# Kernel tuning notes

Measured on AMD Instinct MI355X. Metric: run time of the kernel, lower is better.

Reference implementation:

```python
import jax, jax.numpy as jnp
import numpy as np

MAX = 1e10
H, DK, DV = 16, 64, 64  # heads, key_size, value_size


def setup_inputs() -> dict:
    key = jax.random.key(0)
    ks = jax.random.split(key, 8)
    B, S, D = 2, 2048, 1024
    q = jax.random.normal(ks[0], (B, S, D), dtype=jnp.float32)
    k = jax.random.normal(ks[1], (B, S, D), dtype=jnp.float32)
    v = jax.random.normal(ks[2], (B, S, D), dtype=jnp.float32)
    v_mask = jax.random.randint(ks[3], (B, S), 0, 2, dtype=jnp.int32)
    q_mask = jax.random.randint(ks[4], (B, S), 0, 2, dtype=jnp.int32)
    sc = 1.0 / np.sqrt(D)
    Wq = jax.random.normal(ks[5], (D, H * DK), dtype=jnp.float32) * sc
    Wk = jax.random.normal(ks[6], (D, H * DK), dtype=jnp.float32) * sc
    Wv = jax.random.normal(ks[7], (D, H * DV), dtype=jnp.float32) * sc
    return {"q": q, "k": k, "v": v, "v_mask": v_mask, "q_mask": q_mask,
            "Wq": Wq, "Wk": Wk, "Wv": Wv}


def reference(q, k, v, v_mask, q_mask, Wq, Wk, Wv):
    B, Sq, _ = q.shape
    Sk = k.shape[1]
    # projections -> [B, H, S, d]
    qh = (q @ Wq).reshape(B, Sq, H, DK).transpose(0, 2, 1, 3)
    kh = (k @ Wk).reshape(B, Sk, H, DK).transpose(0, 2, 1, 3)
    vh = (v @ Wv).reshape(B, Sk, H, DV).transpose(0, 2, 1, 3)
    # scores [B, H, Sq, Sk]
    a = jnp.einsum('bhqd,bhkd->bhqk', qh, kh) / np.sqrt(DK).astype(np.float32)
    # additive key-padding mask over key dim
    vm = v_mask.astype(a.dtype)
    a = a - (1.0 - vm)[:, None, None, :] * MAX
    # causal mask (band-part trick)
    causal = jnp.tril(jnp.ones((Sq, Sk), dtype=a.dtype))
    a = a - (1.0 - causal) * MAX
    a = jax.nn.softmax(a, axis=-1)
    out = jnp.einsum('bhqk,bhkd->bqhd', a, vh).reshape(B, Sq, H * DV)
    # multiplicative query-padding mask
    out = out * q_mask.astype(out.dtype)[:, :, None]
    return out
```

## Files before the change

### kernel.cpp

```cpp
#include <hip/hip_runtime.h>
#include <hip/hip_bf16.h>

#define H_    16
#define S_    2048
#define D_    1024
#define MAXV  1e10f

typedef __attribute__((ext_vector_type(8))) short short8;
typedef __attribute__((ext_vector_type(4))) float f32x4;

__device__ __forceinline__ unsigned short f2bf(float f) {
    union { float f; unsigned u; } x; x.f = f;
    unsigned r = x.u + 0x7fffu + ((x.u >> 16) & 1u);
    return (unsigned short)(r >> 16);
}
__device__ __forceinline__ float bf2f(unsigned short h) {
    union { unsigned u; float f; } x; x.u = ((unsigned)h) << 16; return x.f;
}

__global__ __launch_bounds__(256) void scan_kernel(
        const int* __restrict__ vmask, int* __restrict__ cmap,
        int* __restrict__ Jc, int* __restrict__ cumi) {
    int bb = blockIdx.x;
    const int* vm = vmask + (size_t)bb * S_;
    int t = threadIdx.x, lane = t & 63, wave = t >> 6;
    int j0 = t * 8;
    int loc[8], tot = 0;
#pragma unroll
    for (int e = 0; e < 8; e++) { loc[e] = vm[j0 + e] ? 1 : 0; tot += loc[e]; }
    int pre = tot;
#pragma unroll
    for (int d = 1; d < 64; d <<= 1) {
        int x = __shfl_up(pre, d);
        if (lane >= d) pre += x;
    }
    __shared__ int wtot[4];
    if (lane == 63) wtot[wave] = pre;
    __syncthreads();
    int wbase = 0;
    for (int w = 0; w < wave; w++) wbase += wtot[w];
    int run = wbase + pre - tot;
    for (int e = 0; e < 8; e++) {
        int j = j0 + e;
        int before = run;
        run += loc[e];
        cumi[(size_t)bb * S_ + j] = run;
        if (loc[e]) {
            cmap[(size_t)bb * S_ + j] = before;
            Jc[(size_t)bb * S_ + before] = j;
        } else {
            cmap[(size_t)bb * S_ + j] = -1;
        }
    }
    int total = wtot[0] + wtot[1] + wtot[2] + wtot[3];
    for (int c = total + t; c < S_; c += 256) Jc[(size_t)bb * S_ + c] = S_;
}

__global__ __launch_bounds__(256) void wtrans_kernel(
        const float* __restrict__ w0, const float* __restrict__ w1,
        const float* __restrict__ w2, unsigned short* __restrict__ wt) {
    const float* W = blockIdx.z == 0 ? w0 : (blockIdx.z == 1 ? w1 : w2);
    unsigned short* Wt = wt + (size_t)blockIdx.z * (D_ * D_);
    __shared__ float tile[32][33];
    int t = threadIdx.x;
    int k0 = blockIdx.y * 32, n0 = blockIdx.x * 32;
    int r = t >> 3, c4 = (t & 7) * 4;
    float4 v = *(const float4*)&W[(size_t)(k0 + r) * D_ + n0 + c4];
    tile[r][c4 + 0] = v.x; tile[r][c4 + 1] = v.y;
    tile[r][c4 + 2] = v.z; tile[r][c4 + 3] = v.w;
    __syncthreads();
    ushort4 o;
    o.x = f2bf(tile[c4 + 0][r]); o.y = f2bf(tile[c4 + 1][r]);
    o.z = f2bf(tile[c4 + 2][r]); o.w = f2bf(tile[c4 + 3][r]);
    *(ushort4*)&Wt[(size_t)(n0 + r) * D_ + k0 + c4] = o;
}

__global__ __launch_bounds__(256) void conv_kernel(
        const float* __restrict__ q, const float* __restrict__ k,
        const float* __restrict__ v, unsigned short* __restrict__ abf) {
    int z = blockIdx.y;
    const float* src = z == 0 ? q : (z == 1 ? k : v);
    unsigned short* dst = abf + (size_t)z * (4096ull * 1024);
    size_t i = ((size_t)blockIdx.x * 256 + threadIdx.x) * 8;
    float4 f1 = *(const float4*)&src[i];
    float4 f2 = *(const float4*)&src[i + 4];
    short8 o;
    o[0] = (short)f2bf(f1.x); o[1] = (short)f2bf(f1.y);
    o[2] = (short)f2bf(f1.z); o[3] = (short)f2bf(f1.w);
    o[4] = (short)f2bf(f2.x); o[5] = (short)f2bf(f2.y);
    o[6] = (short)f2bf(f2.z); o[7] = (short)f2bf(f2.w);
    *(short8*)&dst[i] = o;
}

template <bool PRE>
__global__ __launch_bounds__(256) void proj_kernel(
        const float* __restrict__ q, const float* __restrict__ k,
        const float* __restrict__ v, const unsigned short* __restrict__ abf,
        const unsigned short* __restrict__ wt, const int* __restrict__ cmap,
        unsigned short* __restrict__ Qh, unsigned short* __restrict__ Kc,
        unsigned short* __restrict__ Vtc) {
    int z = blockIdx.z;
    const float* Af = z == 0 ? q : (z == 1 ? k : v);
    const unsigned short* Ab = abf + (size_t)z * (4096ull * 1024);
    const unsigned short* Bt = wt + (size_t)z * (D_ * D_);
    int m0 = blockIdx.y * 128;
    int n0 = blockIdx.x * 128;
    __shared__ __align__(16) unsigned short As[128][72];
    __shared__ __align__(16) unsigned short Bs[128][72];
    int t = threadIdx.x;
    int wave = t >> 6, lane = t & 63, lg = lane >> 4, lr = lane & 15;
    int wr = (wave >> 1) * 64, wc = (wave & 1) * 64;
    f32x4 acc[4][4];
#pragma unroll
    for (int mi = 0; mi < 4; mi++)
#pragma unroll
        for (int ni = 0; ni < 4; ni++) acc[mi][ni] = (f32x4){0.f, 0.f, 0.f, 0.f};

    int srow = t >> 3, scol = (t & 7) * 8;
    for (int kt = 0; kt < D_ / 64; ++kt) {
        int kk0 = kt * 64;
        __syncthreads();
#pragma unroll
        for (int i = 0; i < 4; i++) {
            int row = i * 32 + srow;
            if (PRE) {
                *(short8*)&As[row][scol] =
                    *(const short8*)&Ab[(size_t)(m0 + row) * D_ + kk0 + scol];
            } else {
                float4 f1 = *(const float4*)&Af[(size_t)(m0 + row) * D_ + kk0 + scol];
                float4 f2 = *(const float4*)&Af[(size_t)(m0 + row) * D_ + kk0 + scol + 4];
                short8 o;
                o[0] = (short)f2bf(f1.x); o[1] = (short)f2bf(f1.y);
                o[2] = (short)f2bf(f1.z); o[3] = (short)f2bf(f1.w);
                o[4] = (short)f2bf(f2.x); o[5] = (short)f2bf(f2.y);
                o[6] = (short)f2bf(f2.z); o[7] = (short)f2bf(f2.w);
                *(short8*)&As[row][scol] = o;
            }
            *(short8*)&Bs[row][scol] =
                *(const short8*)&Bt[(size_t)(n0 + row) * D_ + kk0 + scol];
        }
        __syncthreads();
        short8 af[4][2], bq[4][2];
#pragma unroll
        for (int mi = 0; mi < 4; mi++)
#pragma unroll
            for (int kh = 0; kh < 2; kh++)
                af[mi][kh] = *(const short8*)&As[wr + mi * 16 + lr][kh * 32 + lg * 8];
#pragma unroll
        for (int ni = 0; ni < 4; ni++)
#pragma unroll
            for (int kh = 0; kh < 2; kh++)
                bq[ni][kh] = *(const short8*)&Bs[wc + ni * 16 + lr][kh * 32 + lg * 8];
        __builtin_amdgcn_s_setprio(1);
#pragma unroll
        for (int kh = 0; kh < 2; kh++)
#pragma unroll
            for (int mi = 0; mi < 4; mi++)
#pragma unroll
                for (int ni = 0; ni < 4; ni++)
                    acc[mi][ni] = __builtin_amdgcn_mfma_f32_16x16x32_bf16(
                        af[mi][kh], bq[ni][kh], acc[mi][ni], 0, 0, 0);
        __builtin_amdgcn_s_setprio(0);
    }
    if (z == 0) {
#pragma unroll
        for (int mi = 0; mi < 4; mi++) {
#pragma unroll
            for (int ni = 0; ni < 4; ni++) {
                int col = n0 + wc + ni * 16 + lr;
                int hh = col >> 6, dk = col & 63;
#pragma unroll
                for (int rr = 0; rr < 4; rr++) {
                    int m = m0 + wr + mi * 16 + lg * 4 + rr;
                    int bb = m >> 11, s = m & (S_ - 1);
                    Qh[(((size_t)(bb * H_ + hh)) * S_ + s) * 64 + dk] =
                        f2bf(acc[mi][ni][rr]);
                }
            }
        }
    } else {
        int cm_[4][4], bb_[4][4];
#pragma unroll
        for (int mi = 0; mi < 4; mi++)
#pragma unroll
            for (int rr = 0; rr < 4; rr++) {
                int m = m0 + wr + mi * 16 + lg * 4 + rr;
                int bb = m >> 11, s = m & (S_ - 1);
                bb_[mi][rr] = bb;
                cm_[mi][rr] = cmap[(size_t)bb * S_ + s];
            }
#pragma unroll
        for (int mi = 0; mi < 4; mi++) {
#pragma unroll
            for (int ni = 0; ni < 4; ni++) {
                int col = n0 + wc + ni * 16 + lr;
                int hh = col >> 6, dd = col & 63;
#pragma unroll
                for (int rr = 0; rr < 4; rr++) {
                    int c = cm_[mi][rr];
                    if (c < 0) continue;
                    int bb = bb_[mi][rr];
                    if (z == 1)
                        Kc[(((size_t)(bb * H_ + hh)) * S_ + c) * 64 + dd] =
                            f2bf(acc[mi][ni][rr]);
                    else
                        Vtc[(((size_t)(bb * H_ + hh)) * 64 + dd) * S_ + c] =
                            f2bf(acc[mi][ni][rr]);
                }
            }
        }
    }
}

__global__ __launch_bounds__(256) void attn_kernel(
        const unsigned short* __restrict__ Qh, const unsigned short* __restrict__ Kc,
        const unsigned short* __restrict__ Vtc, const int* __restrict__ Jc,
        const int* __restrict__ cumi, const int* __restrict__ qmask,
        float* __restrict__ out) {
    int pair = blockIdx.x, hh = blockIdx.y, bb = blockIdx.z;
    const unsigned short* Qp = Qh + ((size_t)(bb * H_ + hh)) * S_ * 64;
    const unsigned short* Kp = Kc + ((size_t)(bb * H_ + hh)) * S_ * 64;
    const unsigned short* Vp = Vtc + ((size_t)(bb * H_ + hh)) * 64 * S_;
    const int* Jb = Jc + (size_t)bb * S_;
    int t = threadIdx.x, wave = t >> 6, lane = t & 63, lg = lane >> 4, lr = lane & 15;
    __shared__ __align__(16) unsigned short Ks[64 * 64];
    __shared__ __align__(16) unsigned short Vs[64 * 64];
    __shared__ __align__(16) unsigned short Pl[4][16][72];

    for (int half = 0; half < 2; half++) {
        int qt = half ? (31 - pair) : pair;
        int q0 = qt * 64 + wave * 16;
        int nc = cumi[(size_t)bb * S_ + qt * 64 + 63];
        int nt = (nc + 63) >> 6;
        short8 qf[2];
#pragma unroll
        for (int kh = 0; kh < 2; kh++)
            qf[kh] = *(const short8*)&Qp[(size_t)(q0 + lr) * 64 + kh * 32 + lg * 8];
        f32x4 oacc[4];
#pragma unroll
        for (int ni = 0; ni < 4; ni++) oacc[ni] = (f32x4){0.f, 0.f, 0.f, 0.f};
        float m_run[4], l_run[4];
        int qrow[4];
#pragma unroll
        for (int rr = 0; rr < 4; rr++) {
            m_run[rr] = -__builtin_inff(); l_run[rr] = 0.f;
            qrow[rr] = q0 + lg * 4 + rr;
        }

        for (int kt = 0; kt < nt; ++kt) {
            int kv0 = kt * 64;
            __syncthreads();
#pragma unroll
            for (int i = 0; i < 2; i++) {
                int off = i * 4096 + t * 16;
                int row = off >> 7, colb = off & 127;
                int csw = colb ^ ((row & 7) << 4);
                short8 kkv = *(const short8*)((const char*)Kp + (size_t)(kv0 + row) * 128 + csw);
                short8 vvv = *(const short8*)((const char*)Vp + (size_t)row * 4096 + kv0 * 2 + csw);
                *(short8*)((char*)Ks + off) = kkv;
                *(short8*)((char*)Vs + off) = vvv;
            }
            __syncthreads();
            f32x4 sacc[4];
#pragma unroll
            for (int ni = 0; ni < 4; ni++) sacc[ni] = (f32x4){0.f, 0.f, 0.f, 0.f};
            __builtin_amdgcn_s_setprio(1);
#pragma unroll
            for (int ni = 0; ni < 4; ni++) {
                int row = ni * 16 + lr;
#pragma unroll
                for (int kh = 0; kh < 2; kh++) {
                    int cb = (kh * 64 + lg * 16) ^ ((row & 7) << 4);
                    short8 kf = *(const short8*)((const char*)Ks + row * 128 + cb);
                    sacc[ni] = __builtin_amdgcn_mfma_f32_16x16x32_bf16(qf[kh], kf, sacc[ni], 0, 0, 0);
                }
            }
            __builtin_amdgcn_s_setprio(0);
            float sv[4][4];
#pragma unroll
            for (int ni = 0; ni < 4; ni++) {
                int jo = Jb[kv0 + ni * 16 + lr];
#pragma unroll
                for (int rr = 0; rr < 4; rr++) {
                    float s = sacc[ni][rr] * 0.125f;
                    if (jo > qrow[rr]) s -= MAXV;
                    sv[ni][rr] = s;
                }
            }
            float scl[4];
#pragma unroll
            for (int rr = 0; rr < 4; rr++) {
                float a = fmaxf(fmaxf(sv[0][rr], sv[1][rr]), fmaxf(sv[2][rr], sv[3][rr]));
#pragma unroll
                for (int d = 1; d < 16; d <<= 1) a = fmaxf(a, __shfl_xor(a, d));
                float mn = fmaxf(m_run[rr], a);
                scl[rr] = __expf(m_run[rr] - mn);
                m_run[rr] = mn;
            }
            float pw[4][4], ps[4];
#pragma unroll
            for (int rr = 0; rr < 4; rr++) ps[rr] = 0.f;
#pragma unroll
            for (int ni = 0; ni < 4; ni++)
#pragma unroll
                for (int rr = 0; rr < 4; rr++) {
                    pw[ni][rr] = __expf(sv[ni][rr] - m_run[rr]);
                    ps[rr] += pw[ni][rr];
                }
#pragma unroll
            for (int rr = 0; rr < 4; rr++) {
#pragma unroll
                for (int d = 1; d < 16; d <<= 1) ps[rr] += __shfl_xor(ps[rr], d);
                l_run[rr] = l_run[rr] * scl[rr] + ps[rr];
            }
#pragma unroll
            for (int ni = 0; ni < 4; ni++)
#pragma unroll
                for (int rr = 0; rr < 4; rr++) oacc[ni][rr] *= scl[rr];
#pragma unroll
            for (int ni = 0; ni < 4; ni++)
#pragma unroll
                for (int rr = 0; rr < 4; rr++)
                    Pl[wave][lg * 4 + rr][ni * 16 + lr] = f2bf(pw[ni][rr]);
            short8 pa[2];
#pragma unroll
            for (int kh = 0; kh < 2; kh++)
                pa[kh] = *(const short8*)&Pl[wave][lr][kh * 32 + lg * 8];
            __builtin_amdgcn_s_setprio(1);
#pragma unroll
            for (int ni = 0; ni < 4; ni++) {
                int rowd = ni * 16 + lr;
#pragma unroll
                for (int kh = 0; kh < 2; kh++) {
                    int cb = (kh * 64 + lg * 16) ^ ((rowd & 7) << 4);
                    short8 vf = *(const short8*)((const char*)Vs + rowd * 128 + cb);
                    oacc[ni] = __builtin_amdgcn_mfma_f32_16x16x32_bf16(pa[kh], vf, oacc[ni], 0, 0, 0);
                }
            }
            __builtin_amdgcn_s_setprio(0);
        }
#pragma unroll
        for (int rr = 0; rr < 4; rr++) {
            int qm = qmask[bb * S_ + qrow[rr]];
            float f = (qm != 0 && l_run[rr] > 0.f) ? (float)qm / l_run[rr] : 0.f;
#pragma unroll
            for (int ni = 0; ni < 4; ni++)
                out[((size_t)(bb * S_ + qrow[rr])) * D_ + hh * 64 + ni * 16 + lr] =
                    oacc[ni][rr] * f;
        }
        __syncthreads();
    }
}

__global__ __launch_bounds__(256) void fixup_kernel(
        const int* __restrict__ qmask, const float* __restrict__ v,
        const unsigned short* __restrict__ wt, const unsigned short* __restrict__ Vtc,
        const int* __restrict__ Jc, const int* __restrict__ cumi,
        float* __restrict__ out) {
    int bb = blockIdx.y;
    int p0 = blockIdx.x * 16;
    int t = threadIdx.x;
    int pl = t >> 4, jl = t & 15;
    int d = Jc[(size_t)bb * S_];
    if (d == 0) return;
    int ccount = cumi[(size_t)bb * S_ + S_ - 1];
    int p = p0 + pl;
    int hh = p >> 6, dv = p & 63;
    const unsigned short* vrow = Vtc + ((size_t)(bb * H_ + hh) * 64 + dv) * S_;
    float suf = 0.f;
    for (int c = jl; c < ccount; c += 16) suf += bf2f(vrow[c]);
#pragma unroll
    for (int dd = 1; dd < 16; dd <<= 1) suf += __shfl_xor(suf, dd);
    const unsigned short* wcol = wt + 2ull * D_ * D_ + (size_t)p * D_;
    float pre = 0.f;
    for (int r = 0; r < d; ++r) {
        const float* vr = v + ((size_t)bb * S_ + r) * D_;
        float acc = 0.f;
        for (int kk = jl * 64; kk < jl * 64 + 64; kk += 8) {
            float4 a1 = *(const float4*)&vr[kk];
            float4 a2 = *(const float4*)&vr[kk + 4];
            acc += a1.x * bf2f(wcol[kk + 0]) + a1.y * bf2f(wcol[kk + 1]) +
                   a1.z * bf2f(wcol[kk + 2]) + a1.w * bf2f(wcol[kk + 3]) +
                   a2.x * bf2f(wcol[kk + 4]) + a2.y * bf2f(wcol[kk + 5]) +
                   a2.z * bf2f(wcol[kk + 6]) + a2.w * bf2f(wcol[kk + 7]);
        }
#pragma unroll
        for (int dd = 1; dd < 16; dd <<= 1) acc += __shfl_xor(acc, dd);
        pre += acc;
        if (jl == 0 && qmask[(size_t)bb * S_ + r] != 0)
            out[((size_t)(bb * S_ + r)) * D_ + p] =
                (pre + suf) / (float)(r + 1 + ccount);
    }
}

extern "C" void kernel_launch(void* const* d_in, const int* in_sizes, int n_in,
                              void* d_out, int out_size, void* d_ws, size_t ws_size,
                              hipStream_t stream) {
    const float* q  = (const float*)d_in[0];
    const float* k  = (const float*)d_in[1];
    const float* v  = (const float*)d_in[2];
    const int* vmask = (const int*)d_in[3];
    const int* qmask = (const int*)d_in[4];
    const float* Wq = (const float*)d_in[5];
    const float* Wk = (const float*)d_in[6];
    const float* Wv = (const float*)d_in[7];
    float* out = (float*)d_out;

    char* ws = (char*)d_ws;
    const size_t MB = 1024ull * 1024;
    int* cmap = (int*)ws;
    int* Jc   = (int*)(ws + 16 * 1024);
    int* cumi = (int*)(ws + 32 * 1024);
    unsigned short* Wt  = (unsigned short*)(ws + 64 * 1024);
    unsigned short* Qh  = (unsigned short*)(ws + 64 * 1024 + 6 * MB);
    unsigned short* Kc  = (unsigned short*)(ws + 64 * 1024 + 14 * MB);
    unsigned short* Vtc = (unsigned short*)(ws + 64 * 1024 + 22 * MB);
    unsigned short* Abf = (unsigned short*)(ws + 64 * 1024 + 30 * MB);
    bool pre = ws_size >= 64 * 1024 + 54 * MB;

    scan_kernel<<<dim3(2), 256, 0, stream>>>(vmask, cmap, Jc, cumi);
    wtrans_kernel<<<dim3(32, 32, 3), 256, 0, stream>>>(Wq, Wk, Wv, Wt);
    if (pre) {
        conv_kernel<<<dim3(2048, 3), 256, 0, stream>>>(q, k, v, Abf);
        proj_kernel<true><<<dim3(8, 32, 3), 256, 0, stream>>>(
            q, k, v, Abf, Wt, cmap, Qh, Kc, Vtc);
    } else {
        proj_kernel<false><<<dim3(8, 32, 3), 256, 0, stream>>>(
            q, k, v, Abf, Wt, cmap, Qh, Kc, Vtc);
    }
    attn_kernel<<<dim3(16, H_, 2), 256, 0, stream>>>(Qh, Kc, Vtc, Jc, cumi, qmask, out);
    fixup_kernel<<<dim3(64, 2), 256, 0, stream>>>(qmask, v, Wt, Vtc, Jc, cumi, out);
}
```

Baseline: 214.9 us.

## Register-prefetch next tiles in projection and attention; remap attention grid per XCD

Both the projection GEMM and the attention kernel now load the next K-tile (or K/V tile) from global memory into registers while the current tile is computed, then store it to shared memory at the top of the next iteration. The aim is to hide global load latency behind the MFMA work. The attention kernel also drops the paired causal-balancing loop: it launches one block per query tile in a flat 1024-block grid, mapped so that blocks sharing a (batch, head) land on the same XCD for L2 reuse of K/V. The cost is more live registers, and the per-block causal work is no longer balanced by pairing tiles, so load balance now depends on the scheduler.

```diff
diff --git a/kernel.cpp b/kernel.cpp
--- a/kernel.cpp
+++ b/kernel.cpp
@@ -117,29 +117,50 @@
         for (int ni = 0; ni < 4; ni++) acc[mi][ni] = (f32x4){0.f, 0.f, 0.f, 0.f};
 
     int srow = t >> 3, scol = (t & 7) * 8;
+    short8 aa[4], bb2[4];
+    float4 af_[4][2];
+#pragma unroll
+    for (int i = 0; i < 4; i++) {
+        int row = i * 32 + srow;
+        if (PRE) {
+            aa[i] = *(const short8*)&Ab[(size_t)(m0 + row) * D_ + scol];
+        } else {
+            af_[i][0] = *(const float4*)&Af[(size_t)(m0 + row) * D_ + scol];
+            af_[i][1] = *(const float4*)&Af[(size_t)(m0 + row) * D_ + scol + 4];
+        }
+        bb2[i] = *(const short8*)&Bt[(size_t)(n0 + row) * D_ + scol];
+    }
     for (int kt = 0; kt < D_ / 64; ++kt) {
-        int kk0 = kt * 64;
-        __syncthreads();
 #pragma unroll
         for (int i = 0; i < 4; i++) {
             int row = i * 32 + srow;
             if (PRE) {
-                *(short8*)&As[row][scol] =
-                    *(const short8*)&Ab[(size_t)(m0 + row) * D_ + kk0 + scol];
+                *(short8*)&As[row][scol] = aa[i];
             } else {
-                float4 f1 = *(const float4*)&Af[(size_t)(m0 + row) * D_ + kk0 + scol];
-                float4 f2 = *(const float4*)&Af[(size_t)(m0 + row) * D_ + kk0 + scol + 4];
                 short8 o;
-                o[0] = (short)f2bf(f1.x); o[1] = (short)f2bf(f1.y);
-                o[2] = (short)f2bf(f1.z); o[3] = (short)f2bf(f1.w);
-                o[4] = (short)f2bf(f2.x); o[5] = (short)f2bf(f2.y);
-                o[6] = (short)f2bf(f2.z); o[7] = (short)f2bf(f2.w);
+                o[0] = (short)f2bf(af_[i][0].x); o[1] = (short)f2bf(af_[i][0].y);
+                o[2] = (short)f2bf(af_[i][0].z); o[3] = (short)f2bf(af_[i][0].w);
+                o[4] = (short)f2bf(af_[i][1].x); o[5] = (short)f2bf(af_[i][1].y);
+                o[6] = (short)f2bf(af_[i][1].z); o[7] = (short)f2bf(af_[i][1].w);
                 *(short8*)&As[row][scol] = o;
             }
-            *(short8*)&Bs[row][scol] =
-                *(const short8*)&Bt[(size_t)(n0 + row) * D_ + kk0 + scol];
+            *(short8*)&Bs[row][scol] = bb2[i];
         }
         __syncthreads();
+        if (kt + 1 < D_ / 64) {
+            int kk0 = (kt + 1) * 64;
+#pragma unroll
+            for (int i = 0; i < 4; i++) {
+                int row = i * 32 + srow;
+                if (PRE) {
+                    aa[i] = *(const short8*)&Ab[(size_t)(m0 + row) * D_ + kk0 + scol];
+                } else {
+                    af_[i][0] = *(const float4*)&Af[(size_t)(m0 + row) * D_ + kk0 + scol];
+                    af_[i][1] = *(const float4*)&Af[(size_t)(m0 + row) * D_ + kk0 + scol + 4];
+                }
+                bb2[i] = *(const short8*)&Bt[(size_t)(n0 + row) * D_ + kk0 + scol];
+            }
+        }
         short8 af[4][2], bq[4][2];
 #pragma unroll
         for (int mi = 0; mi < 4; mi++)
@@ -161,6 +182,7 @@
                     acc[mi][ni] = __builtin_amdgcn_mfma_f32_16x16x32_bf16(
                         af[mi][kh], bq[ni][kh], acc[mi][ni], 0, 0, 0);
         __builtin_amdgcn_s_setprio(0);
+        __syncthreads();
     }
     if (z == 0) {
 #pragma unroll
@@ -217,7 +239,11 @@
         const unsigned short* __restrict__ Vtc, const int* __restrict__ Jc,
         const int* __restrict__ cumi, const int* __restrict__ qmask,
         float* __restrict__ out) {
-    int pair = blockIdx.x, hh = blockIdx.y, bb = blockIdx.z;
+    int fid = blockIdx.x;
+    int xcd = fid & 7, slot = fid >> 3;
+    int qt = slot & 31;
+    int g = xcd + 8 * (slot >> 5);
+    int hh = g & 15, bb = g >> 4;
     const unsigned short* Qp = Qh + ((size_t)(bb * H_ + hh)) * S_ * 64;
     const unsigned short* Kp = Kc + ((size_t)(bb * H_ + hh)) * S_ * 64;
     const unsigned short* Vp = Vtc + ((size_t)(bb * H_ + hh)) * 64 * S_;
@@ -227,128 +253,142 @@
     __shared__ __align__(16) unsigned short Vs[64 * 64];
     __shared__ __align__(16) unsigned short Pl[4][16][72];
 
-    for (int half = 0; half < 2; half++) {
-        int qt = half ? (31 - pair) : pair;
-        int q0 = qt * 64 + wave * 16;
-        int nc = cumi[(size_t)bb * S_ + qt * 64 + 63];
-        int nt = (nc + 63) >> 6;
-        short8 qf[2];
+    int q0 = qt * 64 + wave * 16;
+    int nc = cumi[(size_t)bb * S_ + qt * 64 + 63];
+    int nt = (nc + 63) >> 6;
+    short8 qf[2];
+#pragma unroll
+    for (int kh = 0; kh < 2; kh++)
+        qf[kh] = *(const short8*)&Qp[(size_t)(q0 + lr) * 64 + kh * 32 + lg * 8];
+    f32x4 oacc[4];
+#pragma unroll
+    for (int ni = 0; ni < 4; ni++) oacc[ni] = (f32x4){0.f, 0.f, 0.f, 0.f};
+    float m_run[4], l_run[4];
+    int qrow[4];
+#pragma unroll
+    for (int rr = 0; rr < 4; rr++) {
+        m_run[rr] = -__builtin_inff(); l_run[rr] = 0.f;
+        qrow[rr] = q0 + lg * 4 + rr;
+    }
+    int soff[2], srw[2], scsw[2];
+#pragma unroll
+    for (int i = 0; i < 2; i++) {
+        soff[i] = i * 4096 + t * 16;
+        srw[i] = soff[i] >> 7;
+        scsw[i] = (soff[i] & 127) ^ ((srw[i] & 7) << 4);
+    }
+    short8 kreg[2], vreg[2];
+    if (nt > 0) {
+#pragma unroll
+        for (int i = 0; i < 2; i++) {
+            kreg[i] = *(const short8*)((const char*)Kp + (size_t)srw[i] * 128 + scsw[i]);
+            vreg[i] = *(const short8*)((const char*)Vp + (size_t)srw[i] * 4096 + scsw[i]);
+        }
+    }
+
+    for (int kt = 0; kt < nt; ++kt) {
+        int kv0 = kt * 64;
+#pragma unroll
+        for (int i = 0; i < 2; i++) {
+            *(short8*)((char*)Ks + soff[i]) = kreg[i];
+            *(short8*)((char*)Vs + soff[i]) = vreg[i];
+        }
+        __syncthreads();
+        if (kt + 1 < nt) {
+            int kv0n = (kt + 1) * 64;
+#pragma unroll
+            for (int i = 0; i < 2; i++) {
+                kreg[i] = *(const short8*)((const char*)Kp + (size_t)(kv0n + srw[i]) * 128 + scsw[i]);
+                vreg[i] = *(const short8*)((const char*)Vp + (size_t)srw[i] * 4096 + kv0n * 2 + scsw[i]);
+            }
+        }
+        f32x4 sacc[4];
+#pragma unroll
+        for (int ni = 0; ni < 4; ni++) sacc[ni] = (f32x4){0.f, 0.f, 0.f, 0.f};
+        __builtin_amdgcn_s_setprio(1);
+#pragma unroll
+        for (int ni = 0; ni < 4; ni++) {
+            int row = ni * 16 + lr;
+#pragma unroll
+            for (int kh = 0; kh < 2; kh++) {
+                int cb = (kh * 64 + lg * 16) ^ ((row & 7) << 4);
+                short8 kf = *(const short8*)((const char*)Ks + row * 128 + cb);
+                sacc[ni] = __builtin_amdgcn_mfma_f32_16x16x32_bf16(qf[kh], kf, sacc[ni], 0, 0, 0);
+            }
+        }
+        __builtin_amdgcn_s_setprio(0);
+        float sv[4][4];
+#pragma unroll
+        for (int ni = 0; ni < 4; ni++) {
+            int jo = Jb[kv0 + ni * 16 + lr];
+#pragma unroll
+            for (int rr = 0; rr < 4; rr++) {
+                float s = sacc[ni][rr] * 0.125f;
+                if (jo > qrow[rr]) s -= MAXV;
+                sv[ni][rr] = s;
+            }
+        }
+        float scl[4];
+#pragma unroll
+        for (int rr = 0; rr < 4; rr++) {
+            float a = fmaxf(fmaxf(sv[0][rr], sv[1][rr]), fmaxf(sv[2][rr], sv[3][rr]));
+#pragma unroll
+            for (int d = 1; d < 16; d <<= 1) a = fmaxf(a, __shfl_xor(a, d));
+            float mn = fmaxf(m_run[rr], a);
+            scl[rr] = __expf(m_run[rr] - mn);
+            m_run[rr] = mn;
+        }
+        float pw[4][4], ps[4];
+#pragma unroll
+        for (int rr = 0; rr < 4; rr++) ps[rr] = 0.f;
+#pragma unroll
+        for (int ni = 0; ni < 4; ni++)
+#pragma unroll
+            for (int rr = 0; rr < 4; rr++) {
+                pw[ni][rr] = __expf(sv[ni][rr] - m_run[rr]);
+                ps[rr] += pw[ni][rr];
+            }
+#pragma unroll
+        for (int rr = 0; rr < 4; rr++) {
+#pragma unroll
+            for (int d = 1; d < 16; d <<= 1) ps[rr] += __shfl_xor(ps[rr], d);
+            l_run[rr] = l_run[rr] * scl[rr] + ps[rr];
+        }
+#pragma unroll
+        for (int ni = 0; ni < 4; ni++)
+#pragma unroll
+            for (int rr = 0; rr < 4; rr++) oacc[ni][rr] *= scl[rr];
+#pragma unroll
+        for (int ni = 0; ni < 4; ni++)
+#pragma unroll
+            for (int rr = 0; rr < 4; rr++)
+                Pl[wave][lg * 4 + rr][ni * 16 + lr] = f2bf(pw[ni][rr]);
+        short8 pa[2];
 #pragma unroll
         for (int kh = 0; kh < 2; kh++)
-            qf[kh] = *(const short8*)&Qp[(size_t)(q0 + lr) * 64 + kh * 32 + lg * 8];
-        f32x4 oacc[4];
-#pragma unroll
-        for (int ni = 0; ni < 4; ni++) oacc[ni] = (f32x4){0.f, 0.f, 0.f, 0.f};
-        float m_run[4], l_run[4];
-        int qrow[4];
-#pragma unroll
-        for (int rr = 0; rr < 4; rr++) {
-            m_run[rr] = -__builtin_inff(); l_run[rr] = 0.f;
-            qrow[rr] = q0 + lg * 4 + rr;
-        }
-
-        for (int kt = 0; kt < nt; ++kt) {
-            int kv0 = kt * 64;
-            __syncthreads();
-#pragma unroll
-            for (int i = 0; i < 2; i++) {
-                int off = i * 4096 + t * 16;
-                int row = off >> 7, colb = off & 127;
-                int csw = colb ^ ((row & 7) << 4);
-                short8 kkv = *(const short8*)((const char*)Kp + (size_t)(kv0 + row) * 128 + csw);
-                short8 vvv = *(const short8*)((const char*)Vp + (size_t)row * 4096 + kv0 * 2 + csw);
-                *(short8*)((char*)Ks + off) = kkv;
-                *(short8*)((char*)Vs + off) = vvv;
-            }
-            __syncthreads();
-            f32x4 sacc[4];
-#pragma unroll
-            for (int ni = 0; ni < 4; ni++) sacc[ni] = (f32x4){0.f, 0.f, 0.f, 0.f};
-            __builtin_amdgcn_s_setprio(1);
-#pragma unroll
-            for (int ni = 0; ni < 4; ni++) {
-                int row = ni * 16 + lr;
-#pragma unroll
-                for (int kh = 0; kh < 2; kh++) {
-                    int cb = (kh * 64 + lg * 16) ^ ((row & 7) << 4);
-                    short8 kf = *(const short8*)((const char*)Ks + row * 128 + cb);
-                    sacc[ni] = __builtin_amdgcn_mfma_f32_16x16x32_bf16(qf[kh], kf, sacc[ni], 0, 0, 0);
-                }
-            }
-            __builtin_amdgcn_s_setprio(0);
-            float sv[4][4];
-#pragma unroll
-            for (int ni = 0; ni < 4; ni++) {
-                int jo = Jb[kv0 + ni * 16 + lr];
-#pragma unroll
-                for (int rr = 0; rr < 4; rr++) {
-                    float s = sacc[ni][rr] * 0.125f;
-                    if (jo > qrow[rr]) s -= MAXV;
-                    sv[ni][rr] = s;
-                }
-            }
-            float scl[4];
-#pragma unroll
-            for (int rr = 0; rr < 4; rr++) {
-                float a = fmaxf(fmaxf(sv[0][rr], sv[1][rr]), fmaxf(sv[2][rr], sv[3][rr]));
-#pragma unroll
-                for (int d = 1; d < 16; d <<= 1) a = fmaxf(a, __shfl_xor(a, d));
-                float mn = fmaxf(m_run[rr], a);
-                scl[rr] = __expf(m_run[rr] - mn);
-                m_run[rr] = mn;
-            }
-            float pw[4][4], ps[4];
-#pragma unroll
-            for (int rr = 0; rr < 4; rr++) ps[rr] = 0.f;
-#pragma unroll
-            for (int ni = 0; ni < 4; ni++)
-#pragma unroll
-                for (int rr = 0; rr < 4; rr++) {
-                    pw[ni][rr] = __expf(sv[ni][rr] - m_run[rr]);
-                    ps[rr] += pw[ni][rr];
-                }
-#pragma unroll
-            for (int rr = 0; rr < 4; rr++) {
-#pragma unroll
-                for (int d = 1; d < 16; d <<= 1) ps[rr] += __shfl_xor(ps[rr], d);
-                l_run[rr] = l_run[rr] * scl[rr] + ps[rr];
-            }
-#pragma unroll
-            for (int ni = 0; ni < 4; ni++)
-#pragma unroll
-                for (int rr = 0; rr < 4; rr++) oacc[ni][rr] *= scl[rr];
-#pragma unroll
-            for (int ni = 0; ni < 4; ni++)
-#pragma unroll
-                for (int rr = 0; rr < 4; rr++)
-                    Pl[wave][lg * 4 + rr][ni * 16 + lr] = f2bf(pw[ni][rr]);
-            short8 pa[2];
-#pragma unroll
-            for (int kh = 0; kh < 2; kh++)
-                pa[kh] = *(const short8*)&Pl[wave][lr][kh * 32 + lg * 8];
-            __builtin_amdgcn_s_setprio(1);
-#pragma unroll
-            for (int ni = 0; ni < 4; ni++) {
-                int rowd = ni * 16 + lr;
-#pragma unroll
-                for (int kh = 0; kh < 2; kh++) {
-                    int cb = (kh * 64 + lg * 16) ^ ((rowd & 7) << 4);
-                    short8 vf = *(const short8*)((const char*)Vs + rowd * 128 + cb);
-                    oacc[ni] = __builtin_amdgcn_mfma_f32_16x16x32_bf16(pa[kh], vf, oacc[ni], 0, 0, 0);
-                }
-            }
-            __builtin_amdgcn_s_setprio(0);
-        }
-#pragma unroll
-        for (int rr = 0; rr < 4; rr++) {
-            int qm = qmask[bb * S_ + qrow[rr]];
-            float f = (qm != 0 && l_run[rr] > 0.f) ? (float)qm / l_run[rr] : 0.f;
-#pragma unroll
-            for (int ni = 0; ni < 4; ni++)
-                out[((size_t)(bb * S_ + qrow[rr])) * D_ + hh * 64 + ni * 16 + lr] =
-                    oacc[ni][rr] * f;
-        }
+            pa[kh] = *(const short8*)&Pl[wave][lr][kh * 32 + lg * 8];
+        __builtin_amdgcn_s_setprio(1);
+#pragma unroll
+        for (int ni = 0; ni < 4; ni++) {
+            int rowd = ni * 16 + lr;
+#pragma unroll
+            for (int kh = 0; kh < 2; kh++) {
+                int cb = (kh * 64 + lg * 16) ^ ((rowd & 7) << 4);
+                short8 vf = *(const short8*)((const char*)Vs + rowd * 128 + cb);
+                oacc[ni] = __builtin_amdgcn_mfma_f32_16x16x32_bf16(pa[kh], vf, oacc[ni], 0, 0, 0);
+            }
+        }
+        __builtin_amdgcn_s_setprio(0);
         __syncthreads();
+    }
+#pragma unroll
+    for (int rr = 0; rr < 4; rr++) {
+        int qm = qmask[bb * S_ + qrow[rr]];
+        float f = (qm != 0 && l_run[rr] > 0.f) ? (float)qm / l_run[rr] : 0.f;
+#pragma unroll
+        for (int ni = 0; ni < 4; ni++)
+            out[((size_t)(bb * S_ + qrow[rr])) * D_ + hh * 64 + ni * 16 + lr] =
+                oacc[ni][rr] * f;
     }
 }
 
@@ -428,6 +468,6 @@
         proj_kernel<false><<<dim3(8, 32, 3), 256, 0, stream>>>(
             q, k, v, Abf, Wt, cmap, Qh, Kc, Vtc);
     }
-    attn_kernel<<<dim3(16, H_, 2), 256, 0, stream>>>(Qh, Kc, Vtc, Jc, cumi, qmask, out);
+    attn_kernel<<<dim3(1024), 256, 0, stream>>>(Qh, Kc, Vtc, Jc, cumi, qmask, out);
     fixup_kernel<<<dim3(64, 2), 256, 0, stream>>>(qmask, v, Wt, Vtc, Jc, cumi, out);
 }
```

New measurement: 234.9 us. +9.3%, slower.
